# Optimization experiments

Hardware: AMD Instinct MI355X
Metric: run time of the kernel (lower is better)

Reference implementation:

```python
import jax, jax.numpy as jnp
import numpy as np

B, N, T, E, EH, C = 32, 500, 13, 2000, 300, 40
EPS = 1e-5


def _bn_noaffine(x):
    m = x.mean(axis=(0, 2, 3), keepdims=True)
    v = x.var(axis=(0, 2, 3), keepdims=True)
    return (x - m) * jax.lax.rsqrt(v + EPS)


def _bn(x, g, b):
    return g[None, :, None, None] * _bn_noaffine(x) + b[None, :, None, None]


def _conv1x1(x, W, b):
    # x: [B,Cin,N,T], W: [Cout,Cin]
    return jnp.einsum('bcnt,oc->bont', x, W) + b[None, :, None, None]


def _dconv(x, W, b, dil=2):
    # dilated causal conv, kernel (1,2): W [Cout,Cin,2]
    y = jnp.einsum('bcnt,oc->bont', x[..., :-dil], W[:, :, 0])
    y = y + jnp.einsum('bcnt,oc->bont', x[..., dil:], W[:, :, 1])
    return y + b[None, :, None, None]


def setup_inputs() -> dict:
    key = jax.random.key(0)
    ks = jax.random.split(key, 24)
    d = {}
    d['input'] = jax.random.normal(ks[0], (B, 1, N, T), jnp.float32)
    d['A_fwd'] = jax.random.uniform(ks[1], (N, N), jnp.float32) / N
    d['A_bwd'] = jax.random.uniform(ks[2], (N, N), jnp.float32) / N
    d['indices'] = jax.random.randint(ks[3], (2, E), 0, N, jnp.int32)
    d['G0_all'] = jax.random.uniform(ks[4], (E, EH), jnp.float32) * 0.01
    d['G1_all'] = jax.random.uniform(ks[5], (EH, E), jnp.float32) * 0.01
    d['nodevec1'] = jax.random.normal(ks[6], (N, 10), jnp.float32)
    d['nodevec2'] = jax.random.normal(ks[7], (10, N), jnp.float32)
    d['w_edge_f'] = jax.random.uniform(ks[8], (EH,), jnp.float32)
    d['w_edge_b'] = jax.random.uniform(ks[9], (EH,), jnp.float32)
    d['vsrc_f'] = jax.random.normal(ks[10], (3, C), jnp.float32) * 0.05
    d['vdst_f'] = jax.random.normal(ks[11], (3, C), jnp.float32) * 0.05
    d['vsrc_b'] = jax.random.normal(ks[12], (3, C), jnp.float32) * 0.05
    d['vdst_b'] = jax.random.normal(ks[13], (3, C), jnp.float32) * 0.05
    d['start_w'] = jax.random.normal(ks[14], (C, 1), jnp.float32)
    d['start_b'] = jnp.zeros((C,), jnp.float32)
    d['filter_w'] = jax.random.normal(ks[15], (3, C, C, 2), jnp.float32) * (1.0 / np.sqrt(2 * C))
    d['filter_b'] = jnp.zeros((3, C), jnp.float32)
    d['gate_w'] = jax.random.normal(ks[16], (3, C, C, 2), jnp.float32) * (1.0 / np.sqrt(2 * C))
    d['gate_b'] = jnp.zeros((3, C), jnp.float32)
    d['gconv_w'] = jax.random.normal(ks[17], (3, 7 * C, C), jnp.float32) * (1.0 / np.sqrt(7 * C))
    d['gconv_b'] = jnp.zeros((3, C), jnp.float32)
    d['bn_g_gamma'] = jnp.ones((3, C), jnp.float32)
    d['bn_g_beta'] = jnp.zeros((3, C), jnp.float32)
    d['bn_gamma'] = jnp.ones((3, C), jnp.float32)
    d['bn_beta'] = jnp.zeros((3, C), jnp.float32)
    d['skip_w'] = jax.random.normal(ks[18], (3, 320, C), jnp.float32) * (1.0 / np.sqrt(C))
    d['skip_b'] = jnp.zeros((3, 320), jnp.float32)
    d['end1_w'] = jax.random.normal(ks[19], (640, 320), jnp.float32) * (1.0 / np.sqrt(320))
    d['end1_b'] = jnp.zeros((640,), jnp.float32)
    d['end2_w'] = jax.random.normal(ks[20], (12, 640), jnp.float32) * (1.0 / np.sqrt(640))
    d['end2_b'] = jnp.zeros((12,), jnp.float32)
    return d


def reference(input, A_fwd, A_bwd, indices, G0_all, G1_all, nodevec1, nodevec2,
              w_edge_f, w_edge_b, vsrc_f, vdst_f, vsrc_b, vdst_b,
              start_w, start_b, filter_w, filter_b, gate_w, gate_b,
              gconv_w, gconv_b, bn_g_gamma, bn_g_beta, bn_gamma, bn_beta,
              skip_w, skip_b, end1_w, end1_b, end2_w, end2_b):
    x = _bn_noaffine(input)
    x = _conv1x1(x, start_w, start_b)
    b, _, n, _ = x.shape
    # adaptive adjacency: softmax(relu(V1 @ V2)) over rows (torch dim=1 on [N,N])
    adp = jax.nn.softmax(jax.nn.relu(nodevec1 @ nodevec2), axis=1)
    # hypergraph edge-to-edge diffusion operators: G0 @ diag(w) @ G1  ->  [E,E]
    GG_f = G0_all @ (w_edge_f[:, None] * G1_all)
    GG_b = G0_all @ (w_edge_b[:, None] * G1_all)
    i0, i1 = indices[0], indices[1]
    eye = jnp.eye(n, dtype=x.dtype)
    skip = None
    for blk in range(3):
        # dynamic edge scores from node features (mean over time)
        xmean = x.mean(axis=3)                              # [B,C,N]
        src = xmean[:, :, i0]                               # [B,C,E]
        dst = xmean[:, :, i1]
        sc_f = jnp.einsum('bce,c->be', src, vsrc_f[blk]) + jnp.einsum('bce,c->be', dst, vdst_f[blk])
        sc_b = jnp.einsum('bce,c->be', src, vsrc_b[blk]) + jnp.einsum('bce,c->be', dst, vdst_b[blk])
        ef = jax.nn.sigmoid(sc_f @ GG_f)                    # [B,E]
        eb = jax.nn.sigmoid(sc_b @ GG_b)
        # identity medium with sigmoid edge weights scattered at the edge indices
        Mf = jnp.broadcast_to(eye, (b, n, n)).at[:, i0, i1].set(ef)
        Mb = jnp.broadcast_to(eye, (b, n, n)).at[:, i0, i1].set(eb)
        s0 = Mf * A_fwd[None]                               # [B,N,N]
        s1 = jnp.swapaxes(Mb, 1, 2) * A_bwd[None]
        s2 = jnp.broadcast_to(adp, (b, n, n))
        residual = x
        f = jnp.tanh(_dconv(residual, filter_w[blk], filter_b[blk]))
        g = jax.nn.sigmoid(_dconv(residual, gate_w[blk], gate_b[blk]))
        x = f * g
        # diffusion graph conv, order 2, over 3 batched supports
        outs = [x]
        for A in (s0, s1, s2):
            x1 = jnp.einsum('bcnt,bnm->bcmt', x, A)
            outs.append(x1)
            outs.append(jnp.einsum('bcnt,bnm->bcmt', x1, A))
        h = jnp.concatenate(outs, axis=1)                   # [B,7C,N,T']
        x = jnp.einsum('bcnt,co->bont', h, gconv_w[blk]) + gconv_b[blk][None, :, None, None]
        x = _bn(x, bn_g_gamma[blk], bn_g_beta[blk])
        x = x + residual[:, :, :, -x.shape[3]:]
        x = _bn(x, bn_gamma[blk], bn_beta[blk])
        s = _conv1x1(x, skip_w[blk], skip_b[blk])
        skip = s if skip is None else s + skip[:, :, :, -s.shape[3]:]
    x = jax.nn.leaky_relu(skip)
    x = jax.nn.leaky_relu(_conv1x1(x, end1_w, end1_b))
    x = _conv1x1(x, end2_w, end2_b)
    return x
```

## Files before the change

kernel.cpp:

```cpp
#include <hip/hip_runtime.h>
#include <hip/hip_bf16.h>

constexpr int B_  = 32;
constexpr int N_  = 500;
constexpr int T0_ = 13;
constexpr int E_  = 2000;
constexpr int EH_ = 300;
constexpr int C_  = 40;
constexpr float EPS_ = 1e-5f;
constexpr int KP_ = 512;

typedef short bf16x8 __attribute__((ext_vector_type(8)));
typedef _Float16 f16x8 __attribute__((ext_vector_type(8)));
typedef float f32x4  __attribute__((ext_vector_type(4)));

__device__ __forceinline__ float sigm(float x){ return 1.f/(1.f+__expf(-x)); }
__device__ __forceinline__ float lrelu(float x){ return x > 0.f ? x : 0.01f*x; }
__device__ __forceinline__ unsigned short f2bf(float f){
    __hip_bfloat16 h = __float2bfloat16(f);
    return *(unsigned short*)&h;
}

__global__ __launch_bounds__(256) void kern_init(float* __restrict__ insum, int* __restrict__ map,
                                                 int* __restrict__ cnts, int* __restrict__ selfe,
                                                 int* __restrict__ adpTbz)
{
    int i = blockIdx.x*256 + threadIdx.x;
    if (i < 2) insum[i] = 0.f;
    if (i < N_*N_) map[i] = -1;
    if (i < 1024) cnts[i] = 0;
    if (i < 512) selfe[i] = -1;
    if (i < KP_*KP_/2) adpTbz[i] = 0;
}

__global__ __launch_bounds__(256) void kern_zeroacc(float* __restrict__ p, int n)
{
    int i = blockIdx.x*256 + threadIdx.x;
    if (i < n) p[i] = 0.f;
}

__global__ __launch_bounds__(256) void kern_instats(const float* __restrict__ in, float* __restrict__ acc)
{
    float s = 0.f, ss = 0.f;
    int total = B_*N_*T0_;
    for (int i = blockIdx.x*256 + threadIdx.x; i < total; i += gridDim.x*256) {
        float v = in[i]; s += v; ss += v*v;
    }
    __shared__ float l1[256], l2[256];
    l1[threadIdx.x] = s; l2[threadIdx.x] = ss; __syncthreads();
    for (int o = 128; o > 0; o >>= 1) {
        if (threadIdx.x < o) { l1[threadIdx.x] += l1[threadIdx.x+o]; l2[threadIdx.x] += l2[threadIdx.x+o]; }
        __syncthreads();
    }
    if (threadIdx.x == 0) { atomicAdd(&acc[0], l1[0]); atomicAdd(&acc[1], l2[0]); }
}

__global__ __launch_bounds__(256) void kern_x0(const float* __restrict__ in, const float* __restrict__ insum,
    const float* __restrict__ sw, const float* __restrict__ sb, float* __restrict__ x)
{
    int idx = blockIdx.x*256 + threadIdx.x;
    int total = B_*N_*T0_*C_;
    if (idx >= total) return;
    float cnt = (float)(B_*N_*T0_);
    float mean = insum[0]/cnt;
    float var  = insum[1]/cnt - mean*mean;
    float inv  = rsqrtf(var + EPS_);
    int c = idx % C_;
    int pos = idx / C_;
    float xn = (in[pos] - mean)*inv;
    x[idx] = sw[c]*xn + sb[c];
}

__global__ __launch_bounds__(512) void kern_adp(const float* __restrict__ nv1, const float* __restrict__ nv2,
                                                __hip_bfloat16* __restrict__ adpTb)
{
    int n = blockIdx.x;
    int m = threadIdx.x;
    float r = 0.f;
    if (m < N_) {
        #pragma unroll
        for (int k = 0; k < 10; ++k) r += nv1[n*10+k]*nv2[k*N_+m];
        r = r > 0.f ? r : 0.f;
    }
    __shared__ float red[512];
    red[threadIdx.x] = (m < N_) ? r : -1e30f; __syncthreads();
    for (int o = 256; o > 0; o >>= 1) {
        if (threadIdx.x < o) red[threadIdx.x] = fmaxf(red[threadIdx.x], red[threadIdx.x+o]);
        __syncthreads();
    }
    float mx = red[0]; __syncthreads();
    float ev = (m < N_) ? __expf(r - mx) : 0.f;
    red[threadIdx.x] = ev; __syncthreads();
    for (int o = 256; o > 0; o >>= 1) {
        if (threadIdx.x < o) red[threadIdx.x] += red[threadIdx.x+o];
        __syncthreads();
    }
    float sum = red[0];
    if (m < N_) adpTb[(size_t)m*KP_ + n] = __float2bfloat16(ev/sum);
}

__global__ void kern_emax(const int* __restrict__ idx, int* __restrict__ map)
{
    int e = blockIdx.x*256 + threadIdx.x;
    if (e < E_) atomicMax(&map[idx[e]*N_ + idx[E_+e]], e);
}
__global__ void kern_ecnt(const int* __restrict__ idx, const int* __restrict__ map,
                          int* __restrict__ cnt0, int* __restrict__ cnt1, int* __restrict__ selfe)
{
    int e = blockIdx.x*256 + threadIdx.x;
    if (e >= E_) return;
    int i0 = idx[e], i1 = idx[E_+e];
    if (map[i0*N_+i1] != e) return;
    atomicAdd(&cnt1[i1], 1);
    atomicAdd(&cnt0[i0], 1);
    if (i0 == i1) selfe[i0] = e;
}
__global__ __launch_bounds__(512) void kern_scan(const int* __restrict__ cnt0, const int* __restrict__ cnt1,
    int* __restrict__ ptr0, int* __restrict__ ptr1, int* __restrict__ cur0, int* __restrict__ cur1)
{
    __shared__ int s0[512], s1[512];
    int tid = threadIdx.x;
    s0[tid] = (tid < N_) ? cnt0[tid] : 0;
    s1[tid] = (tid < N_) ? cnt1[tid] : 0;
    __syncthreads();
    for (int o = 1; o < 512; o <<= 1) {
        int v0 = (tid >= o) ? s0[tid-o] : 0;
        int v1 = (tid >= o) ? s1[tid-o] : 0;
        __syncthreads();
        s0[tid] += v0; s1[tid] += v1;
        __syncthreads();
    }
    if (tid == 0) { ptr0[0] = 0; ptr1[0] = 0; }
    if (tid < N_) {
        ptr0[tid+1] = s0[tid]; ptr1[tid+1] = s1[tid];
        cur0[tid] = (tid == 0) ? 0 : s0[tid-1];
        cur1[tid] = (tid == 0) ? 0 : s1[tid-1];
    }
}
__global__ void kern_efill(const int* __restrict__ idx, const int* __restrict__ map,
    const float* __restrict__ Af, const float* __restrict__ Ab,
    int* __restrict__ cur0, int* __restrict__ cur1,
    int* __restrict__ e0id, int* __restrict__ e0nb, float* __restrict__ a0v,
    int* __restrict__ e1id, int* __restrict__ e1nb, float* __restrict__ a1v)
{
    int e = blockIdx.x*256 + threadIdx.x;
    if (e >= E_) return;
    int i0 = idx[e], i1 = idx[E_+e];
    if (map[i0*N_+i1] != e) return;
    int s1 = atomicAdd(&cur1[i1], 1);
    e0id[s1] = e; e0nb[s1] = i0; a0v[s1] = Af[i0*N_+i1];
    int s0 = atomicAdd(&cur0[i0], 1);
    e1id[s0] = e; e1nb[s0] = i1; a1v[s0] = Ab[i1*N_+i0];
}

__global__ __launch_bounds__(64) void kern_umean(const float* __restrict__ x, int Tin,
    const float* __restrict__ vsf, const float* __restrict__ vdf,
    const float* __restrict__ vsb, const float* __restrict__ vdb,
    float* __restrict__ usf, float* __restrict__ udf, float* __restrict__ usb, float* __restrict__ udb)
{
    int bn = blockIdx.x;
    const float* xp = x + (size_t)bn*Tin*C_;
    int tid = threadIdx.x;
    float a0=0.f,a1=0.f,a2=0.f,a3=0.f;
    for (int i = tid; i < Tin*C_; i += 64) {
        float v = xp[i]; int c = i % C_;
        a0 += v*vsf[c]; a1 += v*vdf[c]; a2 += v*vsb[c]; a3 += v*vdb[c];
    }
    for (int o = 32; o > 0; o >>= 1) {
        a0 += __shfl_down(a0,o); a1 += __shfl_down(a1,o);
        a2 += __shfl_down(a2,o); a3 += __shfl_down(a3,o);
    }
    if (tid == 0) {
        float inv = 1.f/(float)Tin;
        usf[bn]=a0*inv; udf[bn]=a1*inv; usb[bn]=a2*inv; udb[bn]=a3*inv;
    }
}

__global__ void kern_sc(const int* __restrict__ idx,
    const float* __restrict__ usf, const float* __restrict__ udf,
    const float* __restrict__ usb, const float* __restrict__ udb,
    float* __restrict__ scf, float* __restrict__ scb)
{
    int i = blockIdx.x*256 + threadIdx.x;
    if (i >= B_*E_) return;
    int b = i / E_, e = i % E_;
    int i0 = idx[e], i1 = idx[E_+e];
    scf[i] = usf[b*N_+i0] + udf[b*N_+i1];
    scb[i] = usb[b*N_+i0] + udb[b*N_+i1];
}

__global__ __launch_bounds__(320) void kern_t(const float* __restrict__ scf, const float* __restrict__ scb,
    const float* __restrict__ G0, float* __restrict__ tf, float* __restrict__ tb)
{
    int b = blockIdx.x, chunk = blockIdx.y;
    int e0 = chunk*250;
    __shared__ float sf[250], sb2[250];
    int tid = threadIdx.x;
    for (int i = tid; i < 250; i += 320) { sf[i] = scf[b*E_+e0+i]; sb2[i] = scb[b*E_+e0+i]; }
    __syncthreads();
    if (tid < EH_) {
        float af = 0.f, ab = 0.f;
        for (int i = 0; i < 250; ++i) {
            float g = G0[(size_t)(e0+i)*EH_ + tid];
            af += sf[i]*g; ab += sb2[i]*g;
        }
        atomicAdd(&tf[b*EH_+tid], af);
        atomicAdd(&tb[b*EH_+tid], ab);
    }
}

__global__ __launch_bounds__(256) void kern_ef(const float* __restrict__ tf, const float* __restrict__ tb,
    const float* __restrict__ wf, const float* __restrict__ wb, const float* __restrict__ G1,
    float* __restrict__ ef, float* __restrict__ eb)
{
    int b = blockIdx.y;
    int e = blockIdx.x*256 + threadIdx.x;
    __shared__ float f[EH_], g[EH_];
    for (int i = threadIdx.x; i < EH_; i += 256) {
        f[i] = tf[b*EH_+i]*wf[i];
        g[i] = tb[b*EH_+i]*wb[i];
    }
    __syncthreads();
    if (e < E_) {
        float af = 0.f, ab = 0.f;
        for (int h = 0; h < EH_; ++h) {
            float v = G1[(size_t)h*E_ + e];
            af += f[h]*v; ab += g[h]*v;
        }
        ef[b*E_+e] = sigm(af);
        eb[b*E_+e] = sigm(ab);
    }
}

__global__ __launch_bounds__(256) void kern_dconv_acc(const float* __restrict__ x, int Tin,
    const float* __restrict__ fw, const float* __restrict__ fb4,
    const float* __restrict__ gw, const float* __restrict__ gb4,
    const float* __restrict__ wl0, const float* __restrict__ gbias,
    float* __restrict__ xg, float* __restrict__ gc,
    __hip_bfloat16* __restrict__ xgT, int JP)
{
    int Tout = Tin - 2;
    int nout = Tout*C_;
    int tile = threadIdx.x >> 7;
    int lane = threadIdx.x & 127;
    int bn = blockIdx.x*2 + tile;
    int b = bn / N_, n = bn % N_;
    __shared__ alignas(16) float xs[2][T0_*C_];
    __shared__ alignas(16) float wf[2*C_*C_];
    __shared__ alignas(16) float wg[2*C_*C_];
    __shared__ alignas(16) float wl[C_*C_];
    __shared__ alignas(16) float ps[2][11*C_];
    int tid = threadIdx.x;
    {
        const float4* xp = (const float4*)(x + (size_t)bn*Tin*C_);
        float4* xd = (float4*)xs[tile];
        for (int i = lane; i < (Tin*C_)/4; i += 128) xd[i] = xp[i];
    }
    for (int i = tid; i < 2*C_*C_; i += 256) {
        int k = i / (C_*C_); int r = i % (C_*C_); int c = r / C_; int o = r % C_;
        wf[i] = fw[(o*C_+c)*2 + k];
        wg[i] = gw[(o*C_+c)*2 + k];
    }
    for (int i = tid; i < C_*C_; i += 256) wl[i] = wl0[i];
    __syncthreads();
    int nq = Tout*10;
    for (int u = lane; u < nq; u += 128) {
        int t = u/10, o = (u%10)*4;
        float4 f4 = *(const float4*)&fb4[o];
        float4 g4 = *(const float4*)&gb4[o];
        for (int c = 0; c < C_; ++c) {
            float x0v = xs[tile][t*C_+c], x2v = xs[tile][(t+2)*C_+c];
            float4 wf0 = *(const float4*)&wf[c*C_+o];
            float4 wf1 = *(const float4*)&wf[C_*C_ + c*C_+o];
            float4 wg0 = *(const float4*)&wg[c*C_+o];
            float4 wg1 = *(const float4*)&wg[C_*C_ + c*C_+o];
            f4.x += wf0.x*x0v + wf1.x*x2v;  f4.y += wf0.y*x0v + wf1.y*x2v;
            f4.z += wf0.z*x0v + wf1.z*x2v;  f4.w += wf0.w*x0v + wf1.w*x2v;
            g4.x += wg0.x*x0v + wg1.x*x2v;  g4.y += wg0.y*x0v + wg1.y*x2v;
            g4.z += wg0.z*x0v + wg1.z*x2v;  g4.w += wg0.w*x0v + wg1.w*x2v;
        }
        float4 r4;
        r4.x = tanhf(f4.x)*sigm(g4.x);
        r4.y = tanhf(f4.y)*sigm(g4.y);
        r4.z = tanhf(f4.z)*sigm(g4.z);
        r4.w = tanhf(f4.w)*sigm(g4.w);
        *(float4*)&ps[tile][t*C_+o] = r4;
        *(float4*)&xg[(size_t)bn*nout + t*C_+o] = r4;
        int j = t*C_+o;
        size_t tb = ((size_t)b*JP + j)*KP_ + n;
        xgT[tb]          = __float2bfloat16(r4.x);
        xgT[tb + KP_]    = __float2bfloat16(r4.y);
        xgT[tb + 2*KP_]  = __float2bfloat16(r4.z);
        xgT[tb + 3*KP_]  = __float2bfloat16(r4.w);
    }
    __syncthreads();
    for (int u = lane; u < nq; u += 128) {
        int t = u/10, o = (u%10)*4;
        float4 a4 = *(const float4*)&gbias[o];
        for (int c = 0; c < C_; ++c) {
            float s = ps[tile][t*C_+c];
            float4 w = *(const float4*)&wl[c*C_+o];
            a4.x += s*w.x; a4.y += s*w.y; a4.z += s*w.z; a4.w += s*w.w;
        }
        *(float4*)&gc[(size_t)bn*nout + t*C_+o] = a4;
    }
}

__global__ __launch_bounds__(256) void kern_sparse_acc(const float* __restrict__ in,
    float* __restrict__ outTile, int Tout,
    const int* __restrict__ ptr, const int* __restrict__ nbr, const int* __restrict__ eid,
    const float* __restrict__ aval, const float* __restrict__ coef,
    const float* __restrict__ Amat, const int* __restrict__ selfe,
    const float* __restrict__ gwp, float* __restrict__ gc)
{
    int tile = threadIdx.x >> 7;
    int lane = threadIdx.x & 127;
    int bn = blockIdx.x*2 + tile;
    int b = bn / N_, m = bn % N_;
    __shared__ float wv[2][64];
    __shared__ int   nb[2][64];
    __shared__ alignas(16) float ps[2][11*C_];
    __shared__ alignas(16) float wl[C_*C_];
    int tid = threadIdx.x;
    int p0 = ptr[m], p1 = ptr[m+1];
    int deg = p1 - p0; if (deg > 64) deg = 64;
    if (lane < deg) {
        wv[tile][lane] = coef[b*E_ + eid[p0+lane]] * aval[p0+lane];
        nb[tile][lane] = nbr[p0+lane];
    }
    for (int i = tid; i < C_*C_; i += 256) wl[i] = gwp[i];
    __syncthreads();
    float dval = (selfe[m] >= 0) ? 0.f : Amat[(size_t)m*N_ + m];
    const float* inb = in + (size_t)b*N_*Tout*C_;
    int nout = Tout*C_;
    for (int oi = lane; oi < nout; oi += 128) {
        float acc = dval * inb[(size_t)m*nout + oi];
        for (int j = 0; j < deg; ++j) acc += wv[tile][j]*inb[(size_t)nb[tile][j]*nout + oi];
        ps[tile][oi] = acc;
        if (outTile) outTile[(size_t)bn*nout + oi] = acc;
    }
    __syncthreads();
    int nq = Tout*10;
    for (int u = lane; u < nq; u += 128) {
        int t = u/10, o = (u%10)*4;
        float4 a4 = *(const float4*)&gc[(size_t)bn*nout + t*C_+o];
        for (int c = 0; c < C_; ++c) {
            float s = ps[tile][t*C_+c];
            float4 w = *(const float4*)&wl[c*C_+o];
            a4.x += s*w.x; a4.y += s*w.y; a4.z += s*w.z; a4.w += s*w.w;
        }
        *(float4*)&gc[(size_t)bn*nout + t*C_+o] = a4;
    }
}

__global__ __launch_bounds__(256) void kern_gemm_mfma(const __hip_bfloat16* __restrict__ adpTb,
    const __hip_bfloat16* __restrict__ inT, float* __restrict__ outF,
    __hip_bfloat16* __restrict__ outT, int LD, int JP)
{
    int tid = threadIdx.x;
    int wave = tid >> 6, lane = tid & 63;
    int rn = lane & 15, q = lane >> 4;
    int b = blockIdx.z;
    int m0 = blockIdx.x*64;
    int j0 = blockIdx.y*64;
    const short* Ap = (const short*)adpTb + (size_t)(m0 + wave*16 + rn)*KP_ + q*8;
    const short* Bp = (const short*)inT + ((size_t)b*JP + j0 + rn)*KP_ + q*8;
    f32x4 acc[4] = {};
    for (int k = 0; k < KP_; k += 32) {
        bf16x8 a = *(const bf16x8*)(Ap + k);
        #pragma unroll
        for (int s = 0; s < 4; ++s) {
            bf16x8 bb = *(const bf16x8*)(Bp + (size_t)s*16*KP_ + k);
            acc[s] = __builtin_amdgcn_mfma_f32_16x16x32_bf16(a, bb, acc[s], 0, 0, 0);
        }
    }
    int mb = m0 + wave*16 + q*4;
    #pragma unroll
    for (int s = 0; s < 4; ++s) {
        int j = j0 + s*16 + rn;
        if (j >= LD) continue;
        #pragma unroll
        for (int r = 0; r < 4; ++r) {
            int m = mb + r;
            if (m < N_) outF[((size_t)b*N_ + m)*LD + j] = acc[s][r];
        }
        if (outT) {
            ushort4 v;
            v.x = f2bf(acc[s][0]); v.y = f2bf(acc[s][1]);
            v.z = f2bf(acc[s][2]); v.w = f2bf(acc[s][3]);
            *(ushort4*)((unsigned short*)outT + ((size_t)b*JP + j)*KP_ + mb) = v;
        }
    }
}

__global__ __launch_bounds__(256) void kern_gacc(const float* __restrict__ part, const float* __restrict__ gwp,
    float* __restrict__ gc, int Tout)
{
    int tile = threadIdx.x >> 7;
    int lane = threadIdx.x & 127;
    int bn = blockIdx.x*2 + tile;
    int nout = Tout*C_;
    __shared__ alignas(16) float ps[2][11*C_];
    __shared__ alignas(16) float wl[C_*C_];
    int tid = threadIdx.x;
    {
        const float4* pp = (const float4*)(part + (size_t)bn*nout);
        float4* pd = (float4*)ps[tile];
        for (int i = lane; i < nout/4; i += 128) pd[i] = pp[i];
    }
    for (int i = tid; i < C_*C_; i += 256) wl[i] = gwp[i];
    __syncthreads();
    int nq = Tout*10;
    for (int u = lane; u < nq; u += 128) {
        int t = u/10, o = (u%10)*4;
        float4 a4 = *(const float4*)&gc[(size_t)bn*nout + t*C_+o];
        for (int c = 0; c < C_; ++c) {
            float s = ps[tile][t*C_+c];
            float4 w = *(const float4*)&wl[c*C_+o];
            a4.x += s*w.x; a4.y += s*w.y; a4.z += s*w.z; a4.w += s*w.w;
        }
        *(float4*)&gc[(size_t)bn*nout + t*C_+o] = a4;
    }
}

__global__ __launch_bounds__(320) void kern_bnstats(const float* __restrict__ src, size_t total, float* __restrict__ acc)
{
    int tid = threadIdx.x;
    float s = 0.f, ss = 0.f;
    for (size_t i = (size_t)blockIdx.x*320 + tid; i < total; i += (size_t)gridDim.x*320) {
        float v = src[i]; s += v; ss += v*v;
    }
    __shared__ float ls[320], lss[320];
    ls[tid] = s; lss[tid] = ss; __syncthreads();
    if (tid < C_) {
        float t1 = 0.f, t2 = 0.f;
        for (int r = 0; r < 8; ++r) { t1 += ls[r*C_+tid]; t2 += lss[r*C_+tid]; }
        atomicAdd(&acc[tid], t1); atomicAdd(&acc[C_+tid], t2);
    }
}

__global__ __launch_bounds__(320) void kern_bn1(float* __restrict__ gc, const float* __restrict__ resid,
    int Tin, int Tout, const float* __restrict__ acc1,
    const float* __restrict__ g1, const float* __restrict__ b1, float* __restrict__ acc2)
{
    int tid = threadIdx.x; int c = tid % C_;
    float cnt = (float)(B_*N_*Tout);
    float mean = acc1[c]/cnt;
    float var  = acc1[C_+c]/cnt - mean*mean;
    float inv  = rsqrtf(var + EPS_);
    float gg = g1[c], bb = b1[c];
    int dlt = Tin - Tout;
    float s = 0.f, ss = 0.f;
    size_t total = (size_t)B_*N_*Tout*C_;
    for (size_t i = (size_t)blockIdx.x*320 + tid; i < total; i += (size_t)gridDim.x*320) {
        size_t pos = i / C_; int t = (int)(pos % Tout); size_t bn = pos / Tout;
        float y = gg*(gc[i]-mean)*inv + bb;
        y += resid[(bn*Tin + (t+dlt))*C_ + c];
        gc[i] = y;
        s += y; ss += y*y;
    }
    __shared__ float ls[320], lss[320];
    ls[tid] = s; lss[tid] = ss; __syncthreads();
    if (tid < C_) {
        float t1 = 0.f, t2 = 0.f;
        for (int r = 0; r < 8; ++r) { t1 += ls[r*C_+tid]; t2 += lss[r*C_+tid]; }
        atomicAdd(&acc2[tid], t1); atomicAdd(&acc2[C_+tid], t2);
    }
}

__global__ __launch_bounds__(256) void kern_bn2(const float* __restrict__ gc, float* __restrict__ xout, int Tout,
    const float* __restrict__ acc2, const float* __restrict__ g2, const float* __restrict__ b2)
{
    size_t total = (size_t)B_*N_*Tout*C_;
    size_t i = (size_t)blockIdx.x*256 + threadIdx.x;
    if (i >= total) return;
    int c = (int)(i % C_);
    float cnt = (float)(B_*N_*Tout);
    float mean = acc2[c]/cnt;
    float var  = acc2[C_+c]/cnt - mean*mean;
    float inv  = rsqrtf(var + EPS_);
    xout[i] = g2[c]*(gc[i]-mean)*inv + b2[c];
}

__global__ __launch_bounds__(256) void kern_skip(const float* __restrict__ x, int Tout,
    const float* __restrict__ sw, const float* __restrict__ sbias, __hip_bfloat16* __restrict__ skp, int first)
{
    int bn = blockIdx.x; int half = blockIdx.y;
    int off = Tout - 7;
    __shared__ alignas(16) float xs[7*C_];
    __shared__ alignas(16) float wl[C_*164];
    int tid = threadIdx.x;
    {
        const float4* xp = (const float4*)(x + ((size_t)bn*Tout + off)*C_);
        float4* xd = (float4*)xs;
        for (int i = tid; i < (7*C_)/4; i += 256) xd[i] = xp[i];
    }
    for (int i = tid; i < 160*C_; i += 256) {
        int oo = i / C_, c = i % C_;
        wl[c*164 + oo] = sw[(size_t)(half*160 + oo)*C_ + c];
    }
    __syncthreads();
    for (int u = tid; u < 7*40; u += 256) {
        int t = u / 40, o = (u % 40)*4;
        float4 a4 = {0.f,0.f,0.f,0.f};
        for (int c = 0; c < C_; ++c) {
            float s = xs[t*C_+c];
            float4 w = *(const float4*)&wl[c*164 + o];
            a4.x += s*w.x; a4.y += s*w.y; a4.z += s*w.z; a4.w += s*w.w;
        }
        int og = half*160 + o;
        float4 b4 = *(const float4*)&sbias[og];
        a4.x += b4.x; a4.y += b4.y; a4.z += b4.z; a4.w += b4.w;
        size_t di = ((size_t)bn*7 + t)*320 + og;
        if (first) {
            skp[di+0] = __float2bfloat16(a4.x);
            skp[di+1] = __float2bfloat16(a4.y);
            skp[di+2] = __float2bfloat16(a4.z);
            skp[di+3] = __float2bfloat16(a4.w);
        } else {
            skp[di+0] = __float2bfloat16(__bfloat162float(skp[di+0]) + a4.x);
            skp[di+1] = __float2bfloat16(__bfloat162float(skp[di+1]) + a4.y);
            skp[di+2] = __float2bfloat16(__bfloat162float(skp[di+2]) + a4.z);
            skp[di+3] = __float2bfloat16(__bfloat162float(skp[di+3]) + a4.w);
        }
    }
}

__global__ __launch_bounds__(256) void kern_cvtw(const float* __restrict__ w, __hip_bfloat16* __restrict__ wb, int n)
{
    int i = blockIdx.x*256 + threadIdx.x;
    if (i < n) wb[i] = __float2bfloat16(w[i]);
}

constexpr int AS_ = 328;
__global__ __launch_bounds__(256) void kern_end2(const __hip_bfloat16* __restrict__ skp,
    const __hip_bfloat16* __restrict__ e1wb, const float* __restrict__ e1b,
    const float* __restrict__ e2w, const float* __restrict__ e2b, float* __restrict__ out)
{
    __shared__ short As[64*AS_];
    __shared__ f16x8 w2f[20*64];
    __shared__ _Float16 yw[4][16][36];
    int tid = threadIdx.x;
    int wave = tid >> 6, lane = tid & 63;
    int rn = lane & 15, q = lane >> 4;
    int m0 = blockIdx.x*64;
    for (int i = tid; i < 64*40; i += 256) {
        bf16x8 v = ((const bf16x8*)skp)[(size_t)m0*40 + i];
        bf16x8 r;
        #pragma unroll
        for (int e = 0; e < 8; ++e) {
            unsigned short us = (unsigned short)v[e];
            __hip_bfloat16 h = *(__hip_bfloat16*)&us;
            float f = __bfloat162float(h);
            r[e] = (short)f2bf(lrelu(f));
        }
        int row = i / 40, col = (i % 40)*8;
        *(bf16x8*)&As[row*AS_ + col] = r;
    }
    for (int i = tid; i < 20*64; i += 256) {
        int csp = i >> 6, l = i & 63;
        int o = l & 15, qq = l >> 4;
        f16x8 v;
        #pragma unroll
        for (int e = 0; e < 8; ++e) {
            int c = csp*32 + qq*8 + e;
            v[e] = (o < 12) ? (_Float16)e2w[o*640 + c] : (_Float16)0.f;
        }
        w2f[i] = v;
    }
    __syncthreads();
    bf16x8 areg[10];
    const short* Arow = As + (wave*16 + rn)*AS_ + q*8;
    #pragma unroll
    for (int kk = 0; kk < 10; ++kk) areg[kk] = *(const bf16x8*)(Arow + kk*32);
    f32x4 acc2 = {};
    const short* e1p = (const short*)e1wb;
    for (int cs = 0; cs < 40; ++cs) {
        f32x4 acc = {};
        const short* Bp = e1p + (size_t)(cs*16 + rn)*320 + q*8;
        #pragma unroll
        for (int kk = 0; kk < 10; ++kk) {
            bf16x8 bb = *(const bf16x8*)(Bp + kk*32);
            acc = __builtin_amdgcn_mfma_f32_16x16x32_bf16(areg[kk], bb, acc, 0, 0, 0);
        }
        float bias = e1b[cs*16 + rn];
        int half = (cs & 1)*16;
        #pragma unroll
        for (int r = 0; r < 4; ++r)
            yw[wave][q*4+r][half + rn] = (_Float16)lrelu(acc[r] + bias);
        __builtin_amdgcn_wave_barrier();
        if (cs & 1) {
            f16x8 a2 = *(const f16x8*)&yw[wave][rn][q*8];
            f16x8 b2 = w2f[(cs>>1)*64 + lane];
            acc2 = __builtin_amdgcn_mfma_f32_16x16x32_f16(a2, b2, acc2, 0, 0, 0);
            __builtin_amdgcn_wave_barrier();
        }
    }
    if (rn < 12) {
        float bo = e2b[rn];
        #pragma unroll
        for (int r = 0; r < 4; ++r) {
            int gm = m0 + wave*16 + q*4 + r;
            int t = gm % 7; int bn = gm / 7; int n = bn % N_; int b = bn / N_;
            out[(((size_t)b*12 + rn)*N_ + n)*7 + t] = acc2[r] + bo;
        }
    }
}

extern "C" void kernel_launch(void* const* d_in, const int* in_sizes, int n_in,
                              void* d_out, int out_size, void* d_ws, size_t ws_size,
                              hipStream_t stream)
{
    (void)in_sizes; (void)n_in; (void)out_size;
    const float* input   = (const float*)d_in[0];
    const float* A_fwd   = (const float*)d_in[1];
    const float* A_bwd   = (const float*)d_in[2];
    const int*   indices = (const int*)  d_in[3];
    const float* G0      = (const float*)d_in[4];
    const float* G1      = (const float*)d_in[5];
    const float* nv1     = (const float*)d_in[6];
    const float* nv2     = (const float*)d_in[7];
    const float* wef     = (const float*)d_in[8];
    const float* web     = (const float*)d_in[9];
    const float* vsf     = (const float*)d_in[10];
    const float* vdf     = (const float*)d_in[11];
    const float* vsb     = (const float*)d_in[12];
    const float* vdb     = (const float*)d_in[13];
    const float* start_w = (const float*)d_in[14];
    const float* start_b = (const float*)d_in[15];
    const float* filt_w  = (const float*)d_in[16];
    const float* filt_b  = (const float*)d_in[17];
    const float* gate_w  = (const float*)d_in[18];
    const float* gate_b  = (const float*)d_in[19];
    const float* gcw     = (const float*)d_in[20];
    const float* gcb     = (const float*)d_in[21];
    const float* bng_g   = (const float*)d_in[22];
    const float* bng_b   = (const float*)d_in[23];
    const float* bn_g    = (const float*)d_in[24];
    const float* bn_b    = (const float*)d_in[25];
    const float* skw     = (const float*)d_in[26];
    const float* skb     = (const float*)d_in[27];
    const float* e1w     = (const float*)d_in[28];
    const float* e1b     = (const float*)d_in[29];
    const float* e2w     = (const float*)d_in[30];
    const float* e2b     = (const float*)d_in[31];
    float* out = (float*)d_out;

    float* W = (float*)d_ws;
    size_t off = 0;
    auto FA = [&](size_t n){ off = (off + 3) & ~(size_t)3; float* p = W + off; off += n; return p; };
    float* insum  = FA(2);
    float* tf     = FA((size_t)B_*EH_);
    float* tb     = FA((size_t)B_*EH_);
    float* bnacc1 = FA(80);
    float* bnacc2 = FA(80);
    float* usf = FA((size_t)B_*N_); float* udf = FA((size_t)B_*N_);
    float* usb = FA((size_t)B_*N_); float* udb = FA((size_t)B_*N_);
    float* scf = FA((size_t)B_*E_); float* scb = FA((size_t)B_*E_);
    float* efv = FA((size_t)B_*E_); float* ebv = FA((size_t)B_*E_);
    __hip_bfloat16* adpTb = (__hip_bfloat16*)FA((size_t)KP_*KP_/2);
    float* a0v = FA(E_); float* a1v = FA(E_);
    int* map  = (int*)FA((size_t)N_*N_);
    int* cnt0 = (int*)FA(512); int* cnt1 = (int*)FA(512);
    int* ptr0 = (int*)FA(512); int* ptr1 = (int*)FA(512);
    int* cur0 = (int*)FA(512); int* cur1 = (int*)FA(512);
    int* selfe = (int*)FA(512);
    int* e0id = (int*)FA(E_); int* e0nb = (int*)FA(E_);
    int* e1id = (int*)FA(E_); int* e1nb = (int*)FA(E_);
    float* xA  = FA((size_t)B_*N_*T0_*C_);
    float* xg  = FA((size_t)B_*N_*11*C_);
    float* pa  = FA((size_t)B_*N_*11*C_);
    float* gc  = FA((size_t)B_*N_*11*C_);
    __hip_bfloat16* skp = (__hip_bfloat16*)FA((size_t)B_*N_*7*320/2);
    __hip_bfloat16* xgT = (__hip_bfloat16*)FA((size_t)B_*448*KP_/2);
    __hip_bfloat16* paT = (__hip_bfloat16*)FA((size_t)B_*448*KP_/2);
    __hip_bfloat16* e1wb = (__hip_bfloat16*)xg;

    if (ws_size < off*sizeof(float)) return;

    kern_init<<<(N_*N_+255)/256, 256, 0, stream>>>(insum, map, cnt0, selfe, (int*)adpTb);
    kern_instats<<<256, 256, 0, stream>>>(input, insum);
    kern_x0<<<(B_*N_*T0_*C_+255)/256, 256, 0, stream>>>(input, insum, start_w, start_b, xA);
    kern_adp<<<N_, 512, 0, stream>>>(nv1, nv2, adpTb);
    kern_emax<<<(E_+255)/256, 256, 0, stream>>>(indices, map);
    kern_ecnt<<<(E_+255)/256, 256, 0, stream>>>(indices, map, cnt0, cnt1, selfe);
    kern_scan<<<1, 512, 0, stream>>>(cnt0, cnt1, ptr0, ptr1, cur0, cur1);
    kern_efill<<<(E_+255)/256, 256, 0, stream>>>(indices, map, A_fwd, A_bwd, cur0, cur1,
                                                 e0id, e0nb, a0v, e1id, e1nb, a1v);

    for (int blk = 0; blk < 3; ++blk) {
        int Tin = T0_ - 2*blk;
        int Tout = Tin - 2;
        int LD = Tout*C_;
        int JP = (LD + 63) & ~63;
        size_t total = (size_t)B_*N_*Tout*C_;
        kern_zeroacc<<<(2*B_*EH_+160+255)/256, 256, 0, stream>>>(tf, 2*B_*EH_+160);

        kern_umean<<<B_*N_, 64, 0, stream>>>(xA, Tin, vsf+blk*C_, vdf+blk*C_, vsb+blk*C_, vdb+blk*C_,
                                             usf, udf, usb, udb);
        kern_sc<<<(B_*E_+255)/256, 256, 0, stream>>>(indices, usf, udf, usb, udb, scf, scb);
        kern_t<<<dim3(B_, 8), 320, 0, stream>>>(scf, scb, G0, tf, tb);
        kern_ef<<<dim3(8, B_), 256, 0, stream>>>(tf, tb, wef, web, G1, efv, ebv);

        const float* gwb = gcw + (size_t)blk*7*C_*C_;
        kern_dconv_acc<<<B_*N_/2, 256, 0, stream>>>(xA, Tin,
            filt_w + (size_t)blk*2*C_*C_, filt_b + blk*C_,
            gate_w + (size_t)blk*2*C_*C_, gate_b + blk*C_,
            gwb + 0*C_*C_, gcb + blk*C_, xg, gc, xgT, JP);
        kern_sparse_acc<<<B_*N_/2, 256, 0, stream>>>(xg, pa, Tout, ptr1, e0nb, e0id, a0v, efv,
                                                     A_fwd, selfe, gwb + 1*C_*C_, gc);
        kern_sparse_acc<<<B_*N_/2, 256, 0, stream>>>(pa, nullptr, Tout, ptr1, e0nb, e0id, a0v, efv,
                                                     A_fwd, selfe, gwb + 2*C_*C_, gc);
        kern_sparse_acc<<<B_*N_/2, 256, 0, stream>>>(xg, pa, Tout, ptr0, e1nb, e1id, a1v, ebv,
                                                     A_bwd, selfe, gwb + 3*C_*C_, gc);
        kern_sparse_acc<<<B_*N_/2, 256, 0, stream>>>(pa, nullptr, Tout, ptr0, e1nb, e1id, a1v, ebv,
                                                     A_bwd, selfe, gwb + 4*C_*C_, gc);
        dim3 gg(8, JP/64, B_);
        kern_gemm_mfma<<<gg, 256, 0, stream>>>(adpTb, xgT, pa, paT, LD, JP);
        kern_gacc<<<B_*N_/2, 256, 0, stream>>>(pa, gwb + 5*C_*C_, gc, Tout);
        kern_gemm_mfma<<<gg, 256, 0, stream>>>(adpTb, paT, xg, nullptr, LD, JP);
        kern_gacc<<<B_*N_/2, 256, 0, stream>>>(xg, gwb + 6*C_*C_, gc, Tout);

        kern_bnstats<<<512, 320, 0, stream>>>(gc, total, bnacc1);
        kern_bn1<<<512, 320, 0, stream>>>(gc, xA, Tin, Tout, bnacc1, bng_g + blk*C_, bng_b + blk*C_, bnacc2);
        kern_bn2<<<(int)((total+255)/256), 256, 0, stream>>>(gc, xA, Tout, bnacc2, bn_g + blk*C_, bn_b + blk*C_);

        kern_skip<<<dim3(B_*N_, 2), 256, 0, stream>>>(xA, Tout, skw + (size_t)blk*320*C_, skb + blk*320,
                                                      skp, blk == 0 ? 1 : 0);
    }

    kern_cvtw<<<(640*320+255)/256, 256, 0, stream>>>(e1w, e1wb, 640*320);
    kern_end2<<<B_*N_*7/64, 256, 0, stream>>>(skp, e1wb, e1b, e2w, e2b, out);
}
```

Measured before the change: 2.710 ms.

## Preload A tiles in MFMA GEMM, batch skip conv nodes, restructure end kernel

The adjacency GEMM now loads all 16 A-fragments into registers up front and fully unrolls the K loop, which gives the compiler room to overlap loads. The skip kernel handles four nodes per block, so the transposed weight tile is staged into shared memory once for four nodes instead of once per node. The end kernel reads skip activations straight into registers instead of staging them through LDS, keeps the bias in shared memory, and computes two 16-column output chunks per iteration with split accumulators to raise MFMA-level parallelism. The trade is higher register pressure and fewer blocks in the skip kernel.

```diff
diff --git a/kernel.cpp b/kernel.cpp
--- a/kernel.cpp
+++ b/kernel.cpp
@@ -364,14 +364,17 @@
     int m0 = blockIdx.x*64;
     int j0 = blockIdx.y*64;
     const short* Ap = (const short*)adpTb + (size_t)(m0 + wave*16 + rn)*KP_ + q*8;
+    bf16x8 areg[16];
+    #pragma unroll
+    for (int kk = 0; kk < 16; ++kk) areg[kk] = *(const bf16x8*)(Ap + kk*32);
     const short* Bp = (const short*)inT + ((size_t)b*JP + j0 + rn)*KP_ + q*8;
     f32x4 acc[4] = {};
-    for (int k = 0; k < KP_; k += 32) {
-        bf16x8 a = *(const bf16x8*)(Ap + k);
+    #pragma unroll
+    for (int kk = 0; kk < 16; ++kk) {
         #pragma unroll
         for (int s = 0; s < 4; ++s) {
-            bf16x8 bb = *(const bf16x8*)(Bp + (size_t)s*16*KP_ + k);
-            acc[s] = __builtin_amdgcn_mfma_f32_16x16x32_bf16(a, bb, acc[s], 0, 0, 0);
+            bf16x8 bb = *(const bf16x8*)(Bp + (size_t)s*16*KP_ + kk*32);
+            acc[s] = __builtin_amdgcn_mfma_f32_16x16x32_bf16(areg[kk], bb, acc[s], 0, 0, 0);
         }
     }
     int mb = m0 + wave*16 + q*4;
@@ -485,33 +488,33 @@
 __global__ __launch_bounds__(256) void kern_skip(const float* __restrict__ x, int Tout,
     const float* __restrict__ sw, const float* __restrict__ sbias, __hip_bfloat16* __restrict__ skp, int first)
 {
-    int bn = blockIdx.x; int half = blockIdx.y;
+    int bn0 = blockIdx.x*4; int half = blockIdx.y;
     int off = Tout - 7;
-    __shared__ alignas(16) float xs[7*C_];
+    __shared__ alignas(16) float xs[4][7*C_];
     __shared__ alignas(16) float wl[C_*164];
     int tid = threadIdx.x;
-    {
-        const float4* xp = (const float4*)(x + ((size_t)bn*Tout + off)*C_);
-        float4* xd = (float4*)xs;
-        for (int i = tid; i < (7*C_)/4; i += 256) xd[i] = xp[i];
+    for (int i = tid; i < 4*(7*C_/4); i += 256) {
+        int bl = i / 70, r = i % 70;
+        ((float4*)xs[bl])[r] = ((const float4*)(x + ((size_t)(bn0+bl)*Tout + off)*C_))[r];
     }
     for (int i = tid; i < 160*C_; i += 256) {
         int oo = i / C_, c = i % C_;
         wl[c*164 + oo] = sw[(size_t)(half*160 + oo)*C_ + c];
     }
     __syncthreads();
-    for (int u = tid; u < 7*40; u += 256) {
-        int t = u / 40, o = (u % 40)*4;
+    for (int u = tid; u < 4*7*40; u += 256) {
+        int bl = u / 280; int v = u % 280;
+        int t = v / 40, o = (v % 40)*4;
         float4 a4 = {0.f,0.f,0.f,0.f};
         for (int c = 0; c < C_; ++c) {
-            float s = xs[t*C_+c];
+            float s = xs[bl][t*C_+c];
             float4 w = *(const float4*)&wl[c*164 + o];
             a4.x += s*w.x; a4.y += s*w.y; a4.z += s*w.z; a4.w += s*w.w;
         }
         int og = half*160 + o;
         float4 b4 = *(const float4*)&sbias[og];
         a4.x += b4.x; a4.y += b4.y; a4.z += b4.z; a4.w += b4.w;
-        size_t di = ((size_t)bn*7 + t)*320 + og;
+        size_t di = ((size_t)(bn0+bl)*7 + t)*320 + og;
         if (first) {
             skp[di+0] = __float2bfloat16(a4.x);
             skp[di+1] = __float2bfloat16(a4.y);
@@ -532,31 +535,17 @@
     if (i < n) wb[i] = __float2bfloat16(w[i]);
 }
 
-constexpr int AS_ = 328;
 __global__ __launch_bounds__(256) void kern_end2(const __hip_bfloat16* __restrict__ skp,
     const __hip_bfloat16* __restrict__ e1wb, const float* __restrict__ e1b,
     const float* __restrict__ e2w, const float* __restrict__ e2b, float* __restrict__ out)
 {
-    __shared__ short As[64*AS_];
     __shared__ f16x8 w2f[20*64];
-    __shared__ _Float16 yw[4][16][36];
+    __shared__ _Float16 yw[4][16][40];
+    __shared__ float eb_s[640];
     int tid = threadIdx.x;
     int wave = tid >> 6, lane = tid & 63;
     int rn = lane & 15, q = lane >> 4;
     int m0 = blockIdx.x*64;
-    for (int i = tid; i < 64*40; i += 256) {
-        bf16x8 v = ((const bf16x8*)skp)[(size_t)m0*40 + i];
-        bf16x8 r;
-        #pragma unroll
-        for (int e = 0; e < 8; ++e) {
-            unsigned short us = (unsigned short)v[e];
-            __hip_bfloat16 h = *(__hip_bfloat16*)&us;
-            float f = __bfloat162float(h);
-            r[e] = (short)f2bf(lrelu(f));
-        }
-        int row = i / 40, col = (i % 40)*8;
-        *(bf16x8*)&As[row*AS_ + col] = r;
-    }
     for (int i = tid; i < 20*64; i += 256) {
         int csp = i >> 6, l = i & 63;
         int o = l & 15, qq = l >> 4;
@@ -568,33 +557,50 @@
         }
         w2f[i] = v;
     }
-    __syncthreads();
+    for (int i = tid; i < 640; i += 256) eb_s[i] = e1b[i];
+    const short* Arow = (const short*)skp + (size_t)(m0 + wave*16 + rn)*320 + q*8;
     bf16x8 areg[10];
-    const short* Arow = As + (wave*16 + rn)*AS_ + q*8;
     #pragma unroll
-    for (int kk = 0; kk < 10; ++kk) areg[kk] = *(const bf16x8*)(Arow + kk*32);
+    for (int kk = 0; kk < 10; ++kk) {
+        bf16x8 v = *(const bf16x8*)(Arow + kk*32);
+        bf16x8 r;
+        #pragma unroll
+        for (int e = 0; e < 8; ++e) {
+            unsigned short us = (unsigned short)v[e];
+            __hip_bfloat16 h = *(__hip_bfloat16*)&us;
+            r[e] = (short)f2bf(lrelu(__bfloat162float(h)));
+        }
+        areg[kk] = r;
+    }
+    __syncthreads();
     f32x4 acc2 = {};
     const short* e1p = (const short*)e1wb;
-    for (int cs = 0; cs < 40; ++cs) {
-        f32x4 acc = {};
-        const short* Bp = e1p + (size_t)(cs*16 + rn)*320 + q*8;
+    for (int csp = 0; csp < 20; ++csp) {
+        const short* Bp0 = e1p + (size_t)(csp*32 + rn)*320 + q*8;
+        const short* Bp1 = Bp0 + 16*320;
+        f32x4 c00 = {}, c01 = {}, c10 = {}, c11 = {};
         #pragma unroll
-        for (int kk = 0; kk < 10; ++kk) {
-            bf16x8 bb = *(const bf16x8*)(Bp + kk*32);
-            acc = __builtin_amdgcn_mfma_f32_16x16x32_bf16(areg[kk], bb, acc, 0, 0, 0);
-        }
-        float bias = e1b[cs*16 + rn];
-        int half = (cs & 1)*16;
+        for (int kk = 0; kk < 10; kk += 2) {
+            bf16x8 b00 = *(const bf16x8*)(Bp0 + kk*32);
+            bf16x8 b01 = *(const bf16x8*)(Bp0 + (kk+1)*32);
+            bf16x8 b10 = *(const bf16x8*)(Bp1 + kk*32);
+            bf16x8 b11 = *(const bf16x8*)(Bp1 + (kk+1)*32);
+            c00 = __builtin_amdgcn_mfma_f32_16x16x32_bf16(areg[kk],   b00, c00, 0, 0, 0);
+            c10 = __builtin_amdgcn_mfma_f32_16x16x32_bf16(areg[kk],   b10, c10, 0, 0, 0);
+            c01 = __builtin_amdgcn_mfma_f32_16x16x32_bf16(areg[kk+1], b01, c01, 0, 0, 0);
+            c11 = __builtin_amdgcn_mfma_f32_16x16x32_bf16(areg[kk+1], b11, c11, 0, 0, 0);
+        }
+        float bias0 = eb_s[csp*32 + rn];
+        float bias1 = eb_s[csp*32 + 16 + rn];
         #pragma unroll
-        for (int r = 0; r < 4; ++r)
-            yw[wave][q*4+r][half + rn] = (_Float16)lrelu(acc[r] + bias);
+        for (int r = 0; r < 4; ++r) {
+            yw[wave][q*4+r][rn]      = (_Float16)lrelu(c00[r] + c01[r] + bias0);
+            yw[wave][q*4+r][16 + rn] = (_Float16)lrelu(c10[r] + c11[r] + bias1);
+        }
         __builtin_amdgcn_wave_barrier();
-        if (cs & 1) {
-            f16x8 a2 = *(const f16x8*)&yw[wave][rn][q*8];
-            f16x8 b2 = w2f[(cs>>1)*64 + lane];
-            acc2 = __builtin_amdgcn_mfma_f32_16x16x32_f16(a2, b2, acc2, 0, 0, 0);
-            __builtin_amdgcn_wave_barrier();
-        }
+        f16x8 a2 = *(const f16x8*)&yw[wave][rn][q*8];
+        acc2 = __builtin_amdgcn_mfma_f32_16x16x32_f16(a2, w2f[csp*64 + lane], acc2, 0, 0, 0);
+        __builtin_amdgcn_wave_barrier();
     }
     if (rn < 12) {
         float bo = e2b[rn];
@@ -725,8 +731,8 @@
         kern_bn1<<<512, 320, 0, stream>>>(gc, xA, Tin, Tout, bnacc1, bng_g + blk*C_, bng_b + blk*C_, bnacc2);
         kern_bn2<<<(int)((total+255)/256), 256, 0, stream>>>(gc, xA, Tout, bnacc2, bn_g + blk*C_, bn_b + blk*C_);
 
-        kern_skip<<<dim3(B_*N_, 2), 256, 0, stream>>>(xA, Tout, skw + (size_t)blk*320*C_, skb + blk*320,
-                                                      skp, blk == 0 ? 1 : 0);
+        kern_skip<<<dim3(B_*N_/4, 2), 256, 0, stream>>>(xA, Tout, skw + (size_t)blk*320*C_, skb + blk*320,
+                                                        skp, blk == 0 ? 1 : 0);
     }
 
     kern_cvtw<<<(640*320+255)/256, 256, 0, stream>>>(e1w, e1wb, 640*320);
```

New measurement: 2.609 ms. -3.7%, faster.
